# Performance work log

Measured on AMD Instinct MI355X. Metric: run time of the kernel, lower is better.

The kernel has to match this reference:

```python
import jax, jax.numpy as jnp
import numpy as np

V, L_MAX, D_MODEL, N_LAYER, N_STATE, EXPAND = 49408, 512, 768, 4, 16, 2
D_INNER = EXPAND * D_MODEL            # 1536
DT_RANK = -(-D_MODEL // 16)           # 48 ('auto' = ceil(d_model/16))
D_CONV = 4
B, T = 4, 256
EPS = 1e-5


def setup_inputs() -> dict:
    key = jax.random.key(0)
    ks = jax.random.split(key, 10)
    s = 0.02
    inp = {
        "input_ids": jax.random.randint(ks[0], (B, T), 0, V),
        "emb": jax.random.normal(ks[1], (V, D_MODEL), jnp.float32) * s,
        "pos_emb": jax.random.normal(ks[2], (1, L_MAX, D_MODEL), jnp.float32) * s,
        "in_proj_w": jax.random.normal(ks[3], (N_LAYER, 2 * D_INNER, D_MODEL), jnp.float32) * s,
        "conv_w": jax.random.normal(ks[4], (N_LAYER, D_INNER, D_CONV), jnp.float32) * s,
        "conv_b": jnp.zeros((N_LAYER, D_INNER), jnp.float32),
        "x_proj_w": jax.random.normal(ks[5], (N_LAYER, DT_RANK + 2 * N_STATE, D_INNER), jnp.float32) * s,
        "dt_proj_w": jax.random.normal(ks[6], (N_LAYER, D_INNER, DT_RANK), jnp.float32) * s,
        "dt_proj_b": jnp.full((N_LAYER, D_INNER), -4.6, jnp.float32),  # softplus(-4.6)~0.01, inside [dt_min,dt_max]
        # S4D-real init: A_log[l,d,n] = log(n+1)
        "A_log": jnp.tile(jnp.log(jnp.arange(1, N_STATE + 1, dtype=jnp.float32)), (N_LAYER, D_INNER, 1)),
        "D_skip": jnp.ones((N_LAYER, D_INNER), jnp.float32),
        "out_proj_w": jax.random.normal(ks[7], (N_LAYER, D_MODEL, D_INNER), jnp.float32) * s,
        "norm_w": jnp.ones((D_MODEL,), jnp.float32),
    }
    return inp


def _causal_dwconv(x, w, b):
    # x: (B, C, T), w: (C, K) depthwise, b: (C,) ; causal pad K-1 on the left
    out = jax.lax.conv_general_dilated(
        x, w[:, None, :], window_strides=(1,), padding=[(D_CONV - 1, 0)],
        feature_group_count=x.shape[1], dimension_numbers=("NCH", "OIH", "NCH"))
    return out + b[None, :, None]


def _selective_scan(deltaA, dBx, Cm):
    # deltaA, dBx: (B, T, D, N); Cm: (B, T, N) -> y: (B, T, D)
    def step(h, t_in):
        dA, dbx, c = t_in
        h = dA * h + dbx                          # (B, D, N)
        y = jnp.einsum("bdn,bn->bd", h, c)
        return h, y
    h0 = jnp.zeros(deltaA.shape[:1] + deltaA.shape[2:], deltaA.dtype)
    _, ys = jax.lax.scan(step, h0, (deltaA.swapaxes(0, 1), dBx.swapaxes(0, 1), Cm.swapaxes(0, 1)))
    return ys.swapaxes(0, 1)


def _mamba_block(x, ipw, cw, cb, xpw, dpw, dpb, A_log, Dp, opw):
    # x: (B, T, d_model)
    xz = jnp.einsum("btd,ed->bte", x, ipw)        # (B, T, 2*D_INNER)
    xi, z = jnp.split(xz, 2, axis=-1)
    xi = jax.nn.silu(_causal_dwconv(xi.swapaxes(1, 2), cw, cb)).swapaxes(1, 2)  # (B, T, D_INNER)
    x_dbl = jnp.einsum("btd,ed->bte", xi, xpw)    # (B, T, DT_RANK + 2N)
    dt, Bm, Cm = jnp.split(x_dbl, [DT_RANK, DT_RANK + N_STATE], axis=-1)
    dt = jax.nn.softplus(jnp.einsum("btr,dr->btd", dt, dpw) + dpb)              # (B, T, D_INNER)
    A = -jnp.exp(A_log)                            # (D_INNER, N)
    deltaA = jnp.exp(dt[..., None] * A)            # (B, T, D_INNER, N)
    dBx = dt[..., None] * Bm[:, :, None, :] * xi[..., None]                     # (B, T, D_INNER, N)
    y = _selective_scan(deltaA, dBx, Cm) + Dp * xi
    y = y * jax.nn.silu(z)
    return jnp.einsum("btd,ed->bte", y, opw)       # (B, T, d_model)


def reference(input_ids, emb, pos_emb, in_proj_w, conv_w, conv_b, x_proj_w,
              dt_proj_w, dt_proj_b, A_log, D_skip, out_proj_w, norm_w):
    Tlen = input_ids.shape[1]
    x = emb[input_ids] + pos_emb[:, :Tlen, :]
    for l in range(N_LAYER):
        x = x + _mamba_block(x, in_proj_w[l], conv_w[l], conv_b[l], x_proj_w[l],
                             dt_proj_w[l], dt_proj_b[l], A_log[l], D_skip[l], out_proj_w[l])
    # RMSNormGated with no gate -> plain RMSNorm
    x = x * jax.lax.rsqrt(jnp.mean(x * x, axis=-1, keepdims=True) + EPS) * norm_w
    return x
```

## Files before the change

### kernel.cpp

```cpp
#include <hip/hip_runtime.h>
#include <math.h>

#define TLEN 256
#define BATCH 4
#define DMODEL 768
#define DINNER 1536
#define NSTATE 16
#define DTRANK 48
#define NLAYER 4
#define NTOK 1024

#define S_IP 2359296
#define S_OP 1179648
#define S_XP2 196608
#define WL (S_IP + S_OP + S_XP2)
#define NB_W (WL / 1024)
#define NB_WALL (NB_W * NLAYER)
#define NB_E (NTOK * DMODEL / 256)

typedef __bf16 bf16x8 __attribute__((ext_vector_type(8)));
typedef float f32x4 __attribute__((ext_vector_type(4)));

__device__ inline unsigned short f2b(float f) {
    union { float f; unsigned u; } v;
    v.f = f;
    unsigned r = (v.u + 0x7fffu + ((v.u >> 16) & 1u)) >> 16;
    return (unsigned short)r;
}
__device__ inline float b2f(unsigned short u) {
    union { unsigned u; float f; } v;
    v.u = ((unsigned)u) << 16;
    return v.f;
}

__device__ inline void gload16(const void* g, void* l) {
    __builtin_amdgcn_global_load_lds(
        (const __attribute__((address_space(1))) void*)g,
        (__attribute__((address_space(3))) void*)l, 16, 0, 0);
}

__device__ inline float red16(float p) {
    p += __int_as_float(__builtin_amdgcn_update_dpp(0, __float_as_int(p), 0xB1, 0xf, 0xf, true));
    p += __int_as_float(__builtin_amdgcn_update_dpp(0, __float_as_int(p), 0x4E, 0xf, 0xf, true));
    p += __int_as_float(__builtin_amdgcn_update_dpp(0, __float_as_int(p), 0x124, 0xf, 0xf, true));
    p += __int_as_float(__builtin_amdgcn_update_dpp(0, __float_as_int(p), 0x128, 0xf, 0xf, true));
    return p;
}

__global__ __launch_bounds__(256) void prep_k(const float* __restrict__ ipw,
                                              const float* __restrict__ opw,
                                              const float* __restrict__ xpw,
                                              const int* __restrict__ ids,
                                              const float* __restrict__ emb,
                                              const float* __restrict__ pos,
                                              unsigned short* __restrict__ w_all,
                                              float* __restrict__ x,
                                              unsigned short* __restrict__ xb) {
    int bid = blockIdx.x;
    int tid = threadIdx.x;
    if (bid >= NB_WALL) {
        int idx = (bid - NB_WALL) * 256 + tid;
        int d = idx % DMODEL;
        int bt = idx / DMODEL;
        int t = bt % TLEN;
        float v = emb[(size_t)ids[bt] * DMODEL + d] + pos[t * DMODEL + d];
        x[idx] = v;
        xb[idx] = f2b(v);
        return;
    }
    int l = bid / NB_W;
    int i4 = ((bid % NB_W) * 256 + tid) * 4;
    unsigned short* wl = w_all + (size_t)l * WL;
    if (i4 < S_IP) {
        float4 v = *(const float4*)(ipw + (size_t)l * S_IP + i4);
        ushort4 o; o.x = f2b(v.x); o.y = f2b(v.y); o.z = f2b(v.z); o.w = f2b(v.w);
        *(ushort4*)(wl + i4) = o;
    } else if (i4 < S_IP + S_OP) {
        int i = i4 - S_IP;
        float4 v = *(const float4*)(opw + (size_t)l * S_OP + i);
        ushort4 o; o.x = f2b(v.x); o.y = f2b(v.y); o.z = f2b(v.z); o.w = f2b(v.w);
        *(ushort4*)(wl + S_IP + i) = o;
    } else {
        int i = i4 - S_IP - S_OP;
        int r = i / 1536, k = i % 1536;
        ushort4 o = {0, 0, 0, 0};
        if (r < 80) {
            float4 v = *(const float4*)(xpw + (size_t)l * (80 * 1536) + (size_t)r * 1536 + k);
            o.x = f2b(v.x); o.y = f2b(v.y); o.z = f2b(v.z); o.w = f2b(v.w);
        }
        *(ushort4*)(wl + S_IP + S_OP + i) = o;
    }
}

__global__ __launch_bounds__(256) void ipgemm_k(const unsigned short* __restrict__ A,
                                                const unsigned short* __restrict__ B,
                                                unsigned short* __restrict__ o1) {
    __shared__ __align__(16) unsigned short Ab[3][128 * 64];
    __shared__ __align__(16) unsigned short Bb[3][128 * 64];

    int tid = threadIdx.x;
    int lane = tid & 63;
    int wave = tid >> 6;
    int wm = (wave >> 1) * 64;
    int wn = (wave & 1) * 64;
    int bm = blockIdx.x * 128;
    int bn = blockIdx.y * 128;
    int fr = lane & 15;
    int fq = lane >> 4;
    int fk = fq * 8;
    int srow = lane >> 3;
    int scol = (lane & 7) * 8;
    int gcol = scol ^ (srow << 3);
    int sw = (fr & 7) << 3;

    f32x4 acc[4][4] = {};

    auto stage = [&](int s, int k0) {
#pragma unroll
        for (int c = 0; c < 4; ++c) {
            int r = wave * 32 + c * 8;
            gload16(A + (size_t)(bm + r + srow) * DMODEL + k0 + gcol, &Ab[s][r * 64]);
            gload16(B + (size_t)(bn + r + srow) * DMODEL + k0 + gcol, &Bb[s][r * 64]);
        }
    };

    const int nk = DMODEL / 64;
    stage(0, 0);
    stage(1, 64);

    for (int t = 0; t < nk; ++t) {
        if (t + 1 < nk) {
            asm volatile("s_waitcnt vmcnt(8)" ::: "memory");
        } else {
            asm volatile("s_waitcnt vmcnt(0)" ::: "memory");
        }
        __builtin_amdgcn_s_barrier();
        if (t + 2 < nk) stage((t + 2) % 3, (t + 2) * 64);
        int cur = t % 3;
#pragma unroll
        for (int ks = 0; ks < 2; ++ks) {
            int kk = ks * 32 + fk;
            bf16x8 af[4], bfr[4];
#pragma unroll
            for (int i = 0; i < 4; ++i)
                af[i] = *(const bf16x8*)&Ab[cur][(wm + i * 16 + fr) * 64 + (kk ^ sw)];
#pragma unroll
            for (int j = 0; j < 4; ++j)
                bfr[j] = *(const bf16x8*)&Bb[cur][(wn + j * 16 + fr) * 64 + (kk ^ sw)];
#pragma unroll
            for (int i = 0; i < 4; ++i)
#pragma unroll
                for (int j = 0; j < 4; ++j)
                    acc[i][j] = __builtin_amdgcn_mfma_f32_16x16x32_bf16(
                        af[i], bfr[j], acc[i][j], 0, 0, 0);
        }
        __builtin_amdgcn_s_barrier();
    }

#pragma unroll
    for (int i = 0; i < 4; ++i) {
#pragma unroll
        for (int j = 0; j < 4; ++j) {
            int lc = wn + j * 16 + fr;
#pragma unroll
            for (int q = 0; q < 4; ++q) {
                int lr = wm + i * 16 + fq * 4 + q;
                o1[(size_t)(bm + lr) * NTOK + bn + lc] = f2b(acc[i][j][q]);
            }
        }
    }
}

template <int MODE>
__global__ __launch_bounds__(256) void mgemm_k(const unsigned short* __restrict__ A, int lda,
                                               const unsigned short* __restrict__ B, int ldb,
                                               int K,
                                               float* __restrict__ o0,
                                               unsigned short* __restrict__ o1) {
    __shared__ __align__(16) unsigned short Ab[3][64 * 64];
    __shared__ __align__(16) unsigned short Bb[3][64 * 64];

    int tid = threadIdx.x;
    int lane = tid & 63;
    int wave = tid >> 6;
    int wm = (wave >> 1) * 32;
    int wn = (wave & 1) * 32;
    int bm = blockIdx.x * 64;
    int bn = blockIdx.y * 64;
    int fr = lane & 15;
    int fq = lane >> 4;
    int fk = fq * 8;
    int srow = lane >> 3;
    int scol = (lane & 7) * 8;
    int gcol = scol ^ (srow << 3);
    int sw = (fr & 7) << 3;

    f32x4 acc[2][2] = {};

    auto stage = [&](int s, int k0) {
#pragma unroll
        for (int c = 0; c < 2; ++c) {
            int r = wave * 16 + c * 8;
            gload16(A + (size_t)(bm + r + srow) * lda + k0 + gcol, &Ab[s][r * 64]);
            gload16(B + (size_t)(bn + r + srow) * ldb + k0 + gcol, &Bb[s][r * 64]);
        }
    };

    int nk = K >> 6;
    stage(0, 0);
    stage(1, 64);

    for (int t = 0; t < nk; ++t) {
        if (t + 1 < nk) {
            asm volatile("s_waitcnt vmcnt(4)" ::: "memory");
        } else {
            asm volatile("s_waitcnt vmcnt(0)" ::: "memory");
        }
        __builtin_amdgcn_s_barrier();
        if (t + 2 < nk) stage((t + 2) % 3, (t + 2) * 64);
        int cur = t % 3;
#pragma unroll
        for (int ks = 0; ks < 2; ++ks) {
            int kk = ks * 32 + fk;
            bf16x8 af[2], bfr[2];
#pragma unroll
            for (int i = 0; i < 2; ++i)
                af[i] = *(const bf16x8*)&Ab[cur][(wm + i * 16 + fr) * 64 + (kk ^ sw)];
#pragma unroll
            for (int j = 0; j < 2; ++j)
                bfr[j] = *(const bf16x8*)&Bb[cur][(wn + j * 16 + fr) * 64 + (kk ^ sw)];
#pragma unroll
            for (int i = 0; i < 2; ++i)
#pragma unroll
                for (int j = 0; j < 2; ++j)
                    acc[i][j] = __builtin_amdgcn_mfma_f32_16x16x32_bf16(
                        af[i], bfr[j], acc[i][j], 0, 0, 0);
        }
        __builtin_amdgcn_s_barrier();
    }

#pragma unroll
    for (int i = 0; i < 2; ++i) {
#pragma unroll
        for (int j = 0; j < 2; ++j) {
            int lc = wn + j * 16 + fr;
#pragma unroll
            for (int q = 0; q < 4; ++q) {
                int lr = wm + i * 16 + fq * 4 + q;
                float v = acc[i][j][q];
                if (MODE == 1) {
                    int f = bm + lr;
                    if (f < 80) o0[(size_t)f * NTOK + bn + lc] = v;
                } else {
                    size_t idx = (size_t)(bm + lr) * DMODEL + bn + lc;
                    float nv = o0[idx] + v;
                    o0[idx] = nv;
                    o1[idx] = f2b(nv);
                }
            }
        }
    }
}

__global__ __launch_bounds__(256) void conv_k(const unsigned short* __restrict__ xzT,
                                              const float* __restrict__ cw,
                                              const float* __restrict__ cb,
                                              unsigned short* __restrict__ xib) {
    __shared__ unsigned short tile[4][256];
    int tid = threadIdx.x;
    int ch = tid >> 6;
    int d = blockIdx.x * 4 + ch;
    int b = blockIdx.y;
    int t0 = (tid & 63) * 4;
    const unsigned short* src = xzT + (size_t)d * NTOK + b * TLEN + t0;
    ushort4 cur = *(const ushort4*)src;
    ushort4 prev = {0, 0, 0, 0};
    if (t0 > 0) prev = *(const ushort4*)(src - 4);
    float w0 = cw[d * 4 + 0], w1 = cw[d * 4 + 1], w2 = cw[d * 4 + 2], w3 = cw[d * 4 + 3];
    float bb = cb[d];
    float xw[8] = {b2f(prev.x), b2f(prev.y), b2f(prev.z), b2f(prev.w),
                   b2f(cur.x), b2f(cur.y), b2f(cur.z), b2f(cur.w)};
#pragma unroll
    for (int u = 0; u < 4; ++u) {
        float s = bb + w0 * xw[u + 1] + w1 * xw[u + 2] + w2 * xw[u + 3] + w3 * xw[u + 4];
        float v = s / (1.f + __expf(-s));
        tile[ch][t0 + u] = f2b(v);
    }
    __syncthreads();
    int t = tid;
    ushort4 o;
    o.x = tile[0][t]; o.y = tile[1][t]; o.z = tile[2][t]; o.w = tile[3][t];
    *(ushort4*)(xib + (size_t)(b * TLEN + t) * DINNER + blockIdx.x * 4) = o;
}

__global__ __launch_bounds__(512) void scan_k(const unsigned short* __restrict__ xzT,
                                              const float* __restrict__ xdblT,
                                              const float* __restrict__ dpw,
                                              const float* __restrict__ dpb,
                                              const float* __restrict__ cw,
                                              const float* __restrict__ cb,
                                              const float* __restrict__ Alog,
                                              const float* __restrict__ Dsk,
                                              unsigned short* __restrict__ ybb) {
    __shared__ float dt_s[4][256];
    __shared__ float wdt_s[192];
    __shared__ float yl[4][260];
    __shared__ float cum[4][260];
    __shared__ float hL[8][4][16];
    __shared__ float Pb[8][4][16];
    __shared__ float Hin[8][4][16];

    int tid = threadIdx.x;
    int c = tid >> 6;
    int lane = tid & 63;
    int ch = lane >> 4;
    int n = lane & 15;
    int d0 = blockIdx.x * 4;
    int d = d0 + ch;
    int b = blockIdx.y;
    int tl0 = c * 32;

    if (tid < 192) wdt_s[tid] = dpw[(size_t)d0 * DTRANK + tid];
    __syncthreads();
    {
        int dd = tid >> 7;
        int tt = tid & 127;
        const float* wrow = &wdt_s[dd * DTRANK];
        const float* base = xdblT + (size_t)b * TLEN + tt;
        float a0 = 0.f, a1 = 0.f;
#pragma unroll 8
        for (int k = 0; k < DTRANK; ++k) {
            float w = wrow[k];
            a0 += w * base[(size_t)k * NTOK];
            a1 += w * base[(size_t)k * NTOK + 128];
        }
        float bias = dpb[d0 + dd];
        float v0 = a0 + bias, v1 = a1 + bias;
        v0 = (v0 > 0.f) ? v0 + log1pf(__expf(-v0)) : log1pf(__expf(v0));
        v1 = (v1 > 0.f) ? v1 + log1pf(__expf(-v1)) : log1pf(__expf(v1));
        dt_s[dd][tt] = v0;
        dt_s[dd][tt + 128] = v1;
    }
    __syncthreads();

    float a = -__expf(Alog[(size_t)d * NSTATE + n]);
    float Dv = Dsk[d];
    float w0 = cw[d * 4 + 0], w1 = cw[d * 4 + 1], w2 = cw[d * 4 + 2], w3 = cw[d * 4 + 3];
    float cbv = cb[d];
    const unsigned short* xzp = xzT + (size_t)d * NTOK + b * TLEN + tl0;
    const float* Bp = xdblT + (size_t)(DTRANK + n) * NTOK + b * TLEN + tl0;
    const float* Cp = xdblT + (size_t)(DTRANK + NSTATE + n) * NTOK + b * TLEN + tl0;

    float hm3 = 0.f, hm2 = 0.f, hm1 = 0.f;
    if (tl0 > 0) {
        ushort4 pv = *(const ushort4*)(xzp - 4);
        hm3 = b2f(pv.y); hm2 = b2f(pv.z); hm1 = b2f(pv.w);
    }

    float h = 0.f, cd = 0.f;
    for (int t8 = 0; t8 < 32; t8 += 8) {
        ushort4 xv0 = *(const ushort4*)(xzp + t8), xv1 = *(const ushort4*)(xzp + t8 + 4);
        float4 B0 = *(const float4*)(Bp + t8), B1 = *(const float4*)(Bp + t8 + 4);
        float4 C0 = *(const float4*)(Cp + t8), C1 = *(const float4*)(Cp + t8 + 4);
        float xw[11] = {hm3, hm2, hm1,
                        b2f(xv0.x), b2f(xv0.y), b2f(xv0.z), b2f(xv0.w),
                        b2f(xv1.x), b2f(xv1.y), b2f(xv1.z), b2f(xv1.w)};
        float Bs[8] = {B0.x, B0.y, B0.z, B0.w, B1.x, B1.y, B1.z, B1.w};
        float Cs[8] = {C0.x, C0.y, C0.z, C0.w, C1.x, C1.y, C1.z, C1.w};
#pragma unroll
        for (int u = 0; u < 8; ++u) {
            float sv = cbv + w0 * xw[u] + w1 * xw[u + 1] + w2 * xw[u + 2] + w3 * xw[u + 3];
            float xi = sv / (1.f + __expf(-sv));
            float dtv = dt_s[ch][tl0 + t8 + u];
            cd += dtv;
            float dA = __expf(dtv * a);
            h = dA * h + (dtv * xi) * Bs[u];
            float p = red16(h * Cs[u]);
            if (n == 0) {
                yl[ch][tl0 + t8 + u] = p + Dv * xi;
                cum[ch][tl0 + t8 + u] = cd;
            }
        }
        hm3 = xw[8]; hm2 = xw[9]; hm1 = xw[10];
    }
    hL[c][ch][n] = h;
    Pb[c][ch][n] = __expf(a * cd);
    __syncthreads();
    if (c == 0) {
        float H = 0.f;
        Hin[0][ch][n] = 0.f;
#pragma unroll
        for (int cc = 1; cc < 8; ++cc) {
            H = Pb[cc - 1][ch][n] * H + hL[cc - 1][ch][n];
            Hin[cc][ch][n] = H;
        }
    }
    __syncthreads();
    float Hv = Hin[c][ch][n];
    const unsigned short* zp = xzT + (size_t)(DINNER + d) * NTOK + b * TLEN + tl0;
    for (int t8 = 0; t8 < 32; t8 += 8) {
        float4 C0 = *(const float4*)(Cp + t8), C1 = *(const float4*)(Cp + t8 + 4);
        ushort4 zv0 = *(const ushort4*)(zp + t8), zv1 = *(const ushort4*)(zp + t8 + 4);
        float Cs[8] = {C0.x, C0.y, C0.z, C0.w, C1.x, C1.y, C1.z, C1.w};
        float zs[8] = {b2f(zv0.x), b2f(zv0.y), b2f(zv0.z), b2f(zv0.w),
                       b2f(zv1.x), b2f(zv1.y), b2f(zv1.z), b2f(zv1.w)};
#pragma unroll
        for (int u = 0; u < 8; ++u) {
            float cdt = cum[ch][tl0 + t8 + u];
            float corr = red16(Cs[u] * __expf(a * cdt) * Hv);
            if (n == 0) {
                float y = yl[ch][tl0 + t8 + u] + corr;
                float zz = zs[u];
                y *= zz / (1.f + __expf(-zz));
                yl[ch][tl0 + t8 + u] = y;
            }
        }
    }
    __syncthreads();
    if (tid < 256) {
        int t = tid;
        ushort4 o;
        o.x = f2b(yl[0][t]);
        o.y = f2b(yl[1][t]);
        o.z = f2b(yl[2][t]);
        o.w = f2b(yl[3][t]);
        *(ushort4*)(ybb + (size_t)(b * TLEN + t) * DINNER + blockIdx.x * 4) = o;
    }
}

__global__ __launch_bounds__(256) void rmsnorm_k(const float* __restrict__ x,
                                                 const float* __restrict__ nw,
                                                 float* __restrict__ out) {
    int row = blockIdx.x;
    const float* xr = x + (size_t)row * DMODEL;
    int tid = threadIdx.x;
    float s = 0.f;
    for (int d = tid; d < DMODEL; d += 256) {
        float v = xr[d];
        s += v * v;
    }
#pragma unroll
    for (int off = 32; off >= 1; off >>= 1) s += __shfl_down(s, off);
    __shared__ float red[4];
    __shared__ float scale;
    int wid = tid >> 6, lane = tid & 63;
    if (lane == 0) red[wid] = s;
    __syncthreads();
    if (tid == 0) {
        float tot = red[0] + red[1] + red[2] + red[3];
        scale = rsqrtf(tot / (float)DMODEL + 1e-5f);
    }
    __syncthreads();
    float sc = scale;
    for (int d = tid; d < DMODEL; d += 256)
        out[(size_t)row * DMODEL + d] = xr[d] * sc * nw[d];
}

extern "C" void kernel_launch(void* const* d_in, const int* in_sizes, int n_in,
                              void* d_out, int out_size, void* d_ws, size_t ws_size,
                              hipStream_t stream) {
    const int* ids = (const int*)d_in[0];
    const float* emb = (const float*)d_in[1];
    const float* pos = (const float*)d_in[2];
    const float* ipw = (const float*)d_in[3];
    const float* cw = (const float*)d_in[4];
    const float* cb = (const float*)d_in[5];
    const float* xpw = (const float*)d_in[6];
    const float* dpw = (const float*)d_in[7];
    const float* dpb = (const float*)d_in[8];
    const float* Alog = (const float*)d_in[9];
    const float* Dsk = (const float*)d_in[10];
    const float* opw = (const float*)d_in[11];
    const float* nw = (const float*)d_in[12];

    float* x = (float*)d_ws;
    float* xdblT = x + 786432;
    unsigned short* xb = (unsigned short*)(xdblT + 81920);
    unsigned short* xzT = xb + 786432;
    unsigned short* xib = xzT + 3145728;
    unsigned short* ybb = xib + 1572864;
    unsigned short* w_all = ybb + 1572864;

    prep_k<<<NB_WALL + NB_E, 256, 0, stream>>>(ipw, opw, xpw, ids, emb, pos,
                                               w_all, x, xb);

    for (int l = 0; l < NLAYER; ++l) {
        const unsigned short* w_ip = w_all + (size_t)l * WL;
        const unsigned short* w_op = w_ip + S_IP;
        const unsigned short* w_xp = w_op + S_OP;
        const float* cw_l = cw + (size_t)l * DINNER * 4;
        const float* cb_l = cb + (size_t)l * DINNER;
        const float* dpw_l = dpw + (size_t)l * DINNER * DTRANK;
        const float* dpb_l = dpb + (size_t)l * DINNER;
        const float* Alog_l = Alog + (size_t)l * DINNER * NSTATE;
        const float* Dsk_l = Dsk + (size_t)l * DINNER;

        ipgemm_k<<<dim3(3072 / 128, NTOK / 128), 256, 0, stream>>>(w_ip, xb, xzT);
        conv_k<<<dim3(DINNER / 4, BATCH), 256, 0, stream>>>(xzT, cw_l, cb_l, xib);
        mgemm_k<1><<<dim3(2, NTOK / 64), 256, 0, stream>>>(
            w_xp, DINNER, xib, DINNER, DINNER, xdblT, nullptr);
        scan_k<<<dim3(DINNER / 4, BATCH), 512, 0, stream>>>(
            xzT, xdblT, dpw_l, dpb_l, cw_l, cb_l, Alog_l, Dsk_l, ybb);
        mgemm_k<3><<<dim3(NTOK / 64, DMODEL / 64), 256, 0, stream>>>(
            ybb, DINNER, w_op, DINNER, DINNER, x, xb);
    }

    rmsnorm_k<<<NTOK, 256, 0, stream>>>(x, nw, (float*)d_out);
}
```

Measured before the change: 501.9 us.

## Fuse causal conv+SiLU into split-K x_proj GEMM with atomic accumulation

Removes the separate conv kernel and its xib intermediate by recomputing the depthwise causal conv and SiLU while staging the B tile of a new x_proj GEMM. That GEMM is split along K into six slices and accumulates into xdblT with atomicAdd. xdblT is zeroed inside the in_proj GEMM kernel. This saves one launch and a round trip of the intermediate, at the cost of float atomics, which make results nondeterministic, and a single-buffered GEMM without prefetch.

```diff
diff --git a/kernel.cpp b/kernel.cpp
--- a/kernel.cpp
+++ b/kernel.cpp
@@ -94,11 +94,19 @@
 
 __global__ __launch_bounds__(256) void ipgemm_k(const unsigned short* __restrict__ A,
                                                 const unsigned short* __restrict__ B,
-                                                unsigned short* __restrict__ o1) {
+                                                unsigned short* __restrict__ o1,
+                                                float* __restrict__ xdblT) {
     __shared__ __align__(16) unsigned short Ab[3][128 * 64];
     __shared__ __align__(16) unsigned short Bb[3][128 * 64];
 
     int tid = threadIdx.x;
+    {
+        int unit = (blockIdx.x * gridDim.y + blockIdx.y) * 256 + tid;
+        if (unit < 40960) {
+            float2 z = {0.f, 0.f};
+            *(float2*)(xdblT + unit * 2) = z;
+        }
+    }
     int lane = tid & 63;
     int wave = tid >> 6;
     int wm = (wave >> 1) * 64;
@@ -171,12 +179,107 @@
     }
 }
 
-template <int MODE>
-__global__ __launch_bounds__(256) void mgemm_k(const unsigned short* __restrict__ A, int lda,
-                                               const unsigned short* __restrict__ B, int ldb,
-                                               int K,
-                                               float* __restrict__ o0,
-                                               unsigned short* __restrict__ o1) {
+__global__ __launch_bounds__(256) void xprojf_k(const unsigned short* __restrict__ xzT,
+                                                const unsigned short* __restrict__ w_xp,
+                                                const float* __restrict__ cw,
+                                                const float* __restrict__ cb,
+                                                float* __restrict__ xdblT) {
+    __shared__ __align__(16) unsigned short Ab[128 * 64];
+    __shared__ __align__(16) unsigned short Bb[64 * 64];
+
+    int tid = threadIdx.x;
+    int lane = tid & 63;
+    int wave = tid >> 6;
+    int tok0 = blockIdx.x * 64;
+    int ks = blockIdx.y;
+    int wm = (wave >> 1) * 64;
+    int wn = (wave & 1) * 32;
+    int fr = lane & 15;
+    int fq = lane >> 4;
+    int fk = fq * 8;
+    int srow = lane >> 3;
+    int scol = (lane & 7) * 8;
+    int gcol = scol ^ (srow << 3);
+    int sw = (fr & 7) << 3;
+
+    int tbase = tok0 + wave * 16;
+    bool atStart = ((tbase & 255) == 0);
+
+    f32x4 acc[4][2] = {};
+
+    for (int t = 0; t < 4; ++t) {
+        int k0 = ks * 256 + t * 64;
+#pragma unroll
+        for (int c = 0; c < 4; ++c) {
+            int r = wave * 32 + c * 8;
+            gload16(w_xp + (size_t)(r + srow) * DINNER + k0 + gcol, &Ab[r * 64]);
+        }
+        {
+            int d = k0 + lane;
+            const unsigned short* row = xzT + (size_t)d * NTOK + tbase;
+            ushort4 z4 = {0, 0, 0, 0};
+            ushort4 bl0 = atStart ? z4 : *(const ushort4*)(row - 4);
+            ushort4 bl1 = *(const ushort4*)(row);
+            ushort4 bl2 = *(const ushort4*)(row + 4);
+            ushort4 bl3 = *(const ushort4*)(row + 8);
+            ushort4 bl4 = *(const ushort4*)(row + 12);
+            float4 cw4 = *(const float4*)(cw + d * 4);
+            float cbv = cb[d];
+            float xw[20] = {b2f(bl0.x), b2f(bl0.y), b2f(bl0.z), b2f(bl0.w),
+                            b2f(bl1.x), b2f(bl1.y), b2f(bl1.z), b2f(bl1.w),
+                            b2f(bl2.x), b2f(bl2.y), b2f(bl2.z), b2f(bl2.w),
+                            b2f(bl3.x), b2f(bl3.y), b2f(bl3.z), b2f(bl3.w),
+                            b2f(bl4.x), b2f(bl4.y), b2f(bl4.z), b2f(bl4.w)};
+#pragma unroll
+            for (int u = 0; u < 16; ++u) {
+                float sv = cbv + cw4.x * xw[u + 1] + cw4.y * xw[u + 2] +
+                           cw4.z * xw[u + 3] + cw4.w * xw[u + 4];
+                float v = sv / (1.f + __expf(-sv));
+                int r = wave * 16 + u;
+                Bb[r * 64 + (lane ^ ((u & 7) << 3))] = f2b(v);
+            }
+        }
+        __syncthreads();
+#pragma unroll
+        for (int kss = 0; kss < 2; ++kss) {
+            int kk = kss * 32 + fk;
+            bf16x8 af[4], bfr[2];
+#pragma unroll
+            for (int i = 0; i < 4; ++i)
+                af[i] = *(const bf16x8*)&Ab[(wm + i * 16 + fr) * 64 + (kk ^ sw)];
+#pragma unroll
+            for (int j = 0; j < 2; ++j)
+                bfr[j] = *(const bf16x8*)&Bb[(wn + j * 16 + fr) * 64 + (kk ^ sw)];
+#pragma unroll
+            for (int i = 0; i < 4; ++i)
+#pragma unroll
+                for (int j = 0; j < 2; ++j)
+                    acc[i][j] = __builtin_amdgcn_mfma_f32_16x16x32_bf16(
+                        af[i], bfr[j], acc[i][j], 0, 0, 0);
+        }
+        __syncthreads();
+    }
+
+#pragma unroll
+    for (int i = 0; i < 4; ++i) {
+#pragma unroll
+        for (int j = 0; j < 2; ++j) {
+            int lc = wn + j * 16 + fr;
+#pragma unroll
+            for (int q = 0; q < 4; ++q) {
+                int f = wm + i * 16 + fq * 4 + q;
+                if (f < 80)
+                    atomicAdd(&xdblT[(size_t)f * NTOK + tok0 + lc], acc[i][j][q]);
+            }
+        }
+    }
+}
+
+__global__ __launch_bounds__(256) void opgemm_k(const unsigned short* __restrict__ A, int lda,
+                                                const unsigned short* __restrict__ B, int ldb,
+                                                int K,
+                                                float* __restrict__ o0,
+                                                unsigned short* __restrict__ o1) {
     __shared__ __align__(16) unsigned short Ab[3][64 * 64];
     __shared__ __align__(16) unsigned short Bb[3][64 * 64];
 
@@ -247,50 +350,13 @@
 #pragma unroll
             for (int q = 0; q < 4; ++q) {
                 int lr = wm + i * 16 + fq * 4 + q;
-                float v = acc[i][j][q];
-                if (MODE == 1) {
-                    int f = bm + lr;
-                    if (f < 80) o0[(size_t)f * NTOK + bn + lc] = v;
-                } else {
-                    size_t idx = (size_t)(bm + lr) * DMODEL + bn + lc;
-                    float nv = o0[idx] + v;
-                    o0[idx] = nv;
-                    o1[idx] = f2b(nv);
-                }
+                size_t idx = (size_t)(bm + lr) * DMODEL + bn + lc;
+                float nv = o0[idx] + acc[i][j][q];
+                o0[idx] = nv;
+                o1[idx] = f2b(nv);
             }
         }
     }
-}
-
-__global__ __launch_bounds__(256) void conv_k(const unsigned short* __restrict__ xzT,
-                                              const float* __restrict__ cw,
-                                              const float* __restrict__ cb,
-                                              unsigned short* __restrict__ xib) {
-    __shared__ unsigned short tile[4][256];
-    int tid = threadIdx.x;
-    int ch = tid >> 6;
-    int d = blockIdx.x * 4 + ch;
-    int b = blockIdx.y;
-    int t0 = (tid & 63) * 4;
-    const unsigned short* src = xzT + (size_t)d * NTOK + b * TLEN + t0;
-    ushort4 cur = *(const ushort4*)src;
-    ushort4 prev = {0, 0, 0, 0};
-    if (t0 > 0) prev = *(const ushort4*)(src - 4);
-    float w0 = cw[d * 4 + 0], w1 = cw[d * 4 + 1], w2 = cw[d * 4 + 2], w3 = cw[d * 4 + 3];
-    float bb = cb[d];
-    float xw[8] = {b2f(prev.x), b2f(prev.y), b2f(prev.z), b2f(prev.w),
-                   b2f(cur.x), b2f(cur.y), b2f(cur.z), b2f(cur.w)};
-#pragma unroll
-    for (int u = 0; u < 4; ++u) {
-        float s = bb + w0 * xw[u + 1] + w1 * xw[u + 2] + w2 * xw[u + 3] + w3 * xw[u + 4];
-        float v = s / (1.f + __expf(-s));
-        tile[ch][t0 + u] = f2b(v);
-    }
-    __syncthreads();
-    int t = tid;
-    ushort4 o;
-    o.x = tile[0][t]; o.y = tile[1][t]; o.z = tile[2][t]; o.w = tile[3][t];
-    *(ushort4*)(xib + (size_t)(b * TLEN + t) * DINNER + blockIdx.x * 4) = o;
 }
 
 __global__ __launch_bounds__(512) void scan_k(const unsigned short* __restrict__ xzT,
@@ -477,8 +543,7 @@
     float* xdblT = x + 786432;
     unsigned short* xb = (unsigned short*)(xdblT + 81920);
     unsigned short* xzT = xb + 786432;
-    unsigned short* xib = xzT + 3145728;
-    unsigned short* ybb = xib + 1572864;
+    unsigned short* ybb = xzT + 3145728;
     unsigned short* w_all = ybb + 1572864;
 
     prep_k<<<NB_WALL + NB_E, 256, 0, stream>>>(ipw, opw, xpw, ids, emb, pos,
@@ -495,13 +560,12 @@
         const float* Alog_l = Alog + (size_t)l * DINNER * NSTATE;
         const float* Dsk_l = Dsk + (size_t)l * DINNER;
 
-        ipgemm_k<<<dim3(3072 / 128, NTOK / 128), 256, 0, stream>>>(w_ip, xb, xzT);
-        conv_k<<<dim3(DINNER / 4, BATCH), 256, 0, stream>>>(xzT, cw_l, cb_l, xib);
-        mgemm_k<1><<<dim3(2, NTOK / 64), 256, 0, stream>>>(
-            w_xp, DINNER, xib, DINNER, DINNER, xdblT, nullptr);
+        ipgemm_k<<<dim3(3072 / 128, NTOK / 128), 256, 0, stream>>>(w_ip, xb, xzT, xdblT);
+        xprojf_k<<<dim3(NTOK / 64, 6), 256, 0, stream>>>(
+            xzT, w_xp, cw_l, cb_l, xdblT);
         scan_k<<<dim3(DINNER / 4, BATCH), 512, 0, stream>>>(
             xzT, xdblT, dpw_l, dpb_l, cw_l, cb_l, Alog_l, Dsk_l, ybb);
-        mgemm_k<3><<<dim3(NTOK / 64, DMODEL / 64), 256, 0, stream>>>(
+        opgemm_k<<<dim3(NTOK / 64, DMODEL / 64), 256, 0, stream>>>(
             ybb, DINNER, w_op, DINNER, DINNER, x, xb);
     }
 
```

Result: faster. 449.8 us (-10.4%).
